# Performance work log

Measured on AMD Instinct MI355X. Metric: run time of the kernel, lower is better.

Reference implementation:

```python
import jax, jax.numpy as jnp
import numpy as np

# ---- module config (init_kwargs) ----
B, CIN, H, W_ = 2, 64, 56, 56
COUT, KH, KW = 128, 3, 3
K = CIN * KH * KW               # 576, reduction dim
ARRAY_ROWS = 128
IN_SLICES = (2, 2, 2, 2)        # 8-bit inputs, 2-bit slices
W_SLICES = (2, 2, 2, 2)         # 8-bit weights, 2-bit slices
N_STEPS_IN = 2 ** sum(IN_SLICES)    # 256, unsigned quantizer
N_STEPS_W = 2 ** sum(W_SLICES)      # 256
ADC_BINS = 256
ADC_STEP = 4.0

def _shifts_masks(slices):
    masks, shifts = [], [0]
    for s in slices[::-1]:
        masks.append((1 << s) - 1)
        shifts.append(s + shifts[-1])
    return np.array(shifts[-2::-1], np.int32), np.array(masks[::-1], np.int32)

_ish, _im = _shifts_masks(IN_SLICES)
_wsh, _wm = _shifts_masks(W_SLICES)
ISH, IM = jnp.asarray(_ish), jnp.asarray(_im)
WSH, WM = jnp.asarray(_wsh), jnp.asarray(_wm)
ISF = jnp.asarray((1 << _ish).astype(np.float32))  # slice recombine weights 2^shift
WSF = jnp.asarray((1 << _wsh).astype(np.float32))


def setup_inputs() -> dict:
    key = jax.random.key(0)
    k1, k2 = jax.random.split(key)
    return {
        "x": jax.random.normal(k1, (B, CIN, H, W_), jnp.float32),
        "w": jax.random.normal(k2, (COUT, CIN, KH, KW), jnp.float32),
    }


def _im2col(x):
    # 3x3 SAME conv patches, ordering [Cin, kh, kw] to match w.reshape(COUT, K)
    xp = jnp.pad(x, ((0, 0), (0, 0), (1, 1), (1, 1)))
    cols = jnp.stack([xp[:, :, i:i + H, j:j + W_]
                      for i in range(KH) for j in range(KW)], axis=2)  # [B,Cin,9,H,W]
    return cols.transpose(0, 3, 4, 1, 2).reshape(B * H * W_, K)  # [Nx, K]


def _quant_unsigned(v, n_steps):
    # Quantizer.offset + Quantizer.forward (unsigned, per-row over dim=-1)
    offs = v.min(axis=-1, keepdims=True)
    vr = v - offs
    step = vr.max(axis=-1, keepdims=True) / (n_steps - 1)
    q = jnp.round(jnp.clip(vr, 0.0, step * n_steps) / step).astype(jnp.int32)
    return q, step[..., 0], offs[..., 0]


def _slice_bits(q, shifts, masks):
    # Slicer.forward: stack (q >> shift) & mask along new leading slice dim
    s = shifts.reshape((-1,) + (1,) * q.ndim)
    m = masks.reshape((-1,) + (1,) * q.ndim)
    return (q[None] >> s) & m


def _chunk(t):
    # Chunker.forward over last dim K
    nb = -(-K // ARRAY_ROWS)
    npb = -(-K // nb)
    pad = nb * npb - K
    t = jnp.pad(t, [(0, 0)] * (t.ndim - 1) + [(0, pad)])
    t = t.reshape(t.shape[:-1] + (nb, npb))
    return jnp.moveaxis(t, -2, 0)  # [nb, ..., npb]


def reference(x, w):
    xf = _im2col(x)                    # [Nx, K]
    wf = w.reshape(COUT, K)            # [Ny, K]
    x_sum = xf.sum(axis=-1)            # [Nx]
    w_sum = wf.sum(axis=-1)            # [Ny]

    xq, x_scale, x_offs = _quant_unsigned(xf, N_STEPS_IN)
    wq, w_scale, w_offs = _quant_unsigned(wf, N_STEPS_W)

    xc = _chunk(_slice_bits(xq, ISH, IM))  # [nb, nis, Nx, npb] int32
    wc = _chunk(_slice_bits(wq, WSH, WM))  # [nb, nws, Ny, npb] int32

    # bit-serial crossbar MACs per (chunk, weight-slice, input-slice)
    z = jnp.einsum('bixk,bwyk->bwixy',
                   xc.astype(jnp.float32), wc.astype(jnp.float32))  # [nb,nws,nis,Nx,Ny]

    # ADC digitization (unsigned, fixed step): quantize then dequantize
    z = jnp.round(jnp.clip(z, 0.0, ADC_STEP * ADC_BINS) / ADC_STEP) * ADC_STEP

    # Chunker.reverse: sum crossbar blocks; Slicer.reverse: shift-weighted sums
    z = z.sum(axis=0)                               # [nws,nis,Nx,Ny]
    z = jnp.einsum('wixy,w,i->xy', z, WSF, ISF)     # [Nx,Ny]

    # dequantize scales and unsigned-offset correction:
    # x.y = sx*sy*(xq.yq) + x_offs*sum(y) + y_offs*sum(x) - x_offs*y_offs*K
    z = z * x_scale[:, None] * w_scale[None, :]
    z = (z + x_offs[:, None] * w_sum[None, :]
           + w_offs[None, :] * x_sum[:, None]
           - x_offs[:, None] * w_offs[None, :] * K)

    return z.reshape(B, H, W_, COUT).transpose(0, 3, 1, 2)  # [B,Cout,H,W]
```

## Files before the change

kernel.cpp:

```cpp
#include <hip/hip_runtime.h>


#define KDIM  576
#define NPB   116
#define SSTR  688

typedef int i32x4 __attribute__((ext_vector_type(4)));
typedef float f32x4 __attribute__((ext_vector_type(4)));

__device__ __forceinline__ i32x4 slice2b(i32x4 v, int sh) {
    i32x4 r;
    r[0] = (int)(((unsigned)v[0] >> sh) & 0x03030303u);
    r[1] = (int)(((unsigned)v[1] >> sh) & 0x03030303u);
    r[2] = (int)(((unsigned)v[2] >> sh) & 0x03030303u);
    r[3] = (int)(((unsigned)v[3] >> sh) & 0x03030303u);
    return r;
}

__device__ __forceinline__ void quant36(const float (&v)[36], unsigned char* rowp,
                                        int i16, float* sc, float* of,
                                        float* sm_, int sidx)
{
    float mn = v[0], mx = v[0], sm = 0.f;
#pragma unroll
    for (int m = 0; m < 36; m++) { mn = fminf(mn, v[m]); mx = fmaxf(mx, v[m]); sm += v[m]; }
#pragma unroll
    for (int off = 1; off < 16; off <<= 1) {
        mn = fminf(mn, __shfl_xor(mn, off));
        mx = fmaxf(mx, __shfl_xor(mx, off));
        sm += __shfl_xor(sm, off);
    }
    float step = (mx - mn) / 255.0f;
    if (i16 == 0) { sc[sidx] = step; of[sidx] = mn; sm_[sidx] = sm; }
    int k0 = i16 * 36;
#pragma unroll
    for (int d = 0; d < 9; d++) {
        unsigned int dw = 0;
#pragma unroll
        for (int mb = 0; mb < 4; mb++) {
            int q = (int)rintf((v[d * 4 + mb] - mn) / step);
            q = q < 0 ? 0 : (q > 255 ? 255 : q);
            dw |= (unsigned)q << (8 * mb);
        }
        int kd = k0 + d * 4;
        int ch = kd / NPB;
        *(unsigned int*)(rowp + kd + 12 * ch) = dw;
    }
}

__device__ __forceinline__ void zero_pads(unsigned char* scr, int tid) {
    int rl = tid >> 4, dwp = tid & 15;
    int col = dwp < 12 ? (dwp / 3) * 128 + 116 + (dwp % 3) * 4
                       : 624 + (dwp - 12) * 4;
    *(unsigned int*)(scr + rl * SSTR + col) = 0u;
}

__global__ __launch_bounds__(256) void k_wq(
    const float* __restrict__ w, unsigned char* __restrict__ Wq,
    float* __restrict__ wsc, float* __restrict__ wof, float* __restrict__ wsm)
{
    __shared__ __align__(16) unsigned char scrW[16 * SSTR];
    int tid = threadIdx.x, wv = tid >> 6, lane = tid & 63;
    int g = lane >> 4, i16 = lane & 15;
    int ctile = blockIdx.x;

    zero_pads(scrW, tid);
    __syncthreads();

    int rl = wv * 4 + g;
    int row = ctile * 16 + rl;
    const float* wr = w + (size_t)row * KDIM + i16 * 36;
    float v[36];
#pragma unroll
    for (int d = 0; d < 9; d++) {
        f32x4 t = *(const f32x4*)(wr + d * 4);
        v[d*4+0] = t[0]; v[d*4+1] = t[1]; v[d*4+2] = t[2]; v[d*4+3] = t[3];
    }
    quant36(v, scrW + rl * SSTR, i16, wsc, wof, wsm, row);
    __syncthreads();

    for (int idx = tid; idx < 640; idx += 256)
        *(i32x4*)(Wq + (size_t)ctile * 10240 + idx * 16) =
            *(const i32x4*)(scrW + (idx & 15) * SSTR + (idx >> 4) * 16);
}

__global__ __launch_bounds__(256) void k_main(
    const float* __restrict__ x, const unsigned char* __restrict__ Wq,
    const float* __restrict__ wscg, const float* __restrict__ wofg,
    const float* __restrict__ wsmg, float* __restrict__ out)
{
    __shared__ float xs2[64 * 57];
    __shared__ __align__(16) unsigned char scrX[16 * SSTR];
    __shared__ float xsc[16], xof[16], xsm[16];

    int tid = threadIdx.x, wv = tid >> 6, lane = tid & 63;
    int g = lane >> 4, i16 = lane & 15;
    int blk = blockIdx.x;
    int rtile = blk >> 1, chalf = blk & 1;
    int b = rtile >= 196 ? 1 : 0;
    int pos0 = (rtile - 196 * b) * 16;
    const float* xb = x + (size_t)(b * 64) * 3136;

    for (int i = tid; i < 64 * 54; i += 256) {
        int cin = i / 54, rem = i - cin * 54;
        int kh = rem / 18;
        int gg = pos0 + (rem - kh * 18) - 1;
        float vv = 0.f;
        if (gg >= 0 && gg < 3136) {
            int hg = gg / 56, wg = gg - hg * 56;
            int r = hg - 1 + kh;
            if (r >= 0 && r < 56) vv = xb[cin * 3136 + r * 56 + wg];
        }
        xs2[cin * 57 + rem] = vv;
    }
    zero_pads(scrX, tid);
    __syncthreads();

    {
        int i = wv * 4 + g;
        int pos = pos0 + i;
        int w_ = pos - (pos / 56) * 56;
        float v[36];
#pragma unroll
        for (int m = 0; m < 36; m++) {
            int r9 = m % 9, kh = r9 / 3, kw = r9 - kh * 3;
            int cin = i16 * 4 + m / 9;
            int ww = w_ - 1 + kw;
            v[m] = (ww >= 0 && ww < 56) ? xs2[cin * 57 + kh * 18 + i + kw] : 0.f;
        }
        quant36(v, scrX + i * SSTR, i16, xsc, xof, xsm, i);
    }
    __syncthreads();

    int ctl = chalf * 4 + wv;
    const unsigned char* Wg = Wq + (size_t)ctl * 10240;
    const unsigned char* xp = scrX + i16 * SSTR + g * 16;

    i32x4 acc = {0, 0, 0, 0};
    const i32x4 zero = {0, 0, 0, 0};

    for (int chunk = 0; chunk < 5; chunk++) {
        i32x4 ar0 = *(const i32x4*)(xp + chunk * 128);
        i32x4 ar1 = *(const i32x4*)(xp + chunk * 128 + 64);
        const i32x4* Wp = (const i32x4*)(Wg + chunk * 2048) + lane;
        i32x4 br0 = Wp[0], br1 = Wp[64];

        i32x4 wsl[4][2];
#pragma unroll
        for (int ws = 0; ws < 4; ws++) {
            wsl[ws][0] = slice2b(br0, 6 - 2 * ws);
            wsl[ws][1] = slice2b(br1, 6 - 2 * ws);
        }
#pragma unroll
        for (int is = 0; is < 4; is++) {
            int ish = 6 - 2 * is;
            i32x4 b0 = slice2b(ar0, ish);
            i32x4 b1 = slice2b(ar1, ish);
#pragma unroll
            for (int ws = 0; ws < 4; ws++) {
                i32x4 d = __builtin_amdgcn_mfma_i32_16x16x64_i8(wsl[ws][0], b0, zero, 0, 0, 0);
                d = __builtin_amdgcn_mfma_i32_16x16x64_i8(wsl[ws][1], b1, d, 0, 0, 0);
                int sh = ish + (6 - 2 * ws);
#pragma unroll
                for (int r = 0; r < 4; r++) {
                    int z = d[r];
                    z = z > 1024 ? 1024 : z;
                    int r4 = (z + 1 + ((z >> 2) & 1)) & ~3;
                    acc[r] += r4 << sh;
                }
            }
        }
    }

    float xs = xsc[i16], xo = xof[i16], xsmv = xsm[i16];
    int hw = pos0 + i16;
#pragma unroll
    for (int r = 0; r < 4; r++) {
        int wrow = ctl * 16 + g * 4 + r;
        float tt = ((float)acc[r] * xs) * wscg[wrow];
        float res = ((tt + xo * wsmg[wrow]) + wofg[wrow] * xsmv)
                  - (xo * wofg[wrow]) * 576.0f;
        out[(size_t)(b * 128 + wrow) * 3136 + hw] = res;
    }
}

extern "C" void kernel_launch(void* const* d_in, const int* in_sizes, int n_in,
                              void* d_out, int out_size, void* d_ws, size_t ws_size,
                              hipStream_t stream) {
    const float* x = (const float*)d_in[0];
    const float* w = (const float*)d_in[1];
    float* out = (float*)d_out;

    unsigned char* Wq = (unsigned char*)d_ws;
    float* wsc = (float*)(Wq + 81920);
    float* wof = wsc + 128;
    float* wsm = wof + 128;

    hipLaunchKernelGGL(k_wq, dim3(8), dim3(256), 0, stream, w, Wq, wsc, wof, wsm);
    hipLaunchKernelGGL(k_main, dim3(784), dim3(256), 0, stream,
                       x, Wq, wsc, wof, wsm, out);
}
```

Measured before the change: 40.00 us.

## Fuse weight quantization into main kernel and split K across waves

Removes the separate weight-quantization kernel launch. Each block now quantizes its own 32 weight rows into shared memory, reusing the input staging buffer. The grid grows to four output-channel quarters per row tile, and pairs of waves split the five K-chunks, combining partial sums through shared memory. Chunks are interleaved two at a time to raise MFMA independence. The cost is redundant weight loading and quantization in every block (1568 blocks, each rereading 32 rows of fp32 weights), plus an extra barrier.

```diff
diff --git a/kernel.cpp b/kernel.cpp
--- a/kernel.cpp
+++ b/kernel.cpp
@@ -17,6 +17,17 @@
     return r;
 }
 
+__device__ __forceinline__ void adc_acc(const i32x4 d, int sh, i32x4& acc) {
+#pragma unroll
+    for (int r = 0; r < 4; r++) {
+        int z = d[r];
+        z = z > 1024 ? 1024 : z;
+        int t = (z >> 2) & 1;
+        int r4 = (z + 1 + t) & ~3;
+        acc[r] += r4 << sh;
+    }
+}
+
 __device__ __forceinline__ void quant36(const float (&v)[36], unsigned char* rowp,
                                         int i16, float* sc, float* of,
                                         float* sm_, int sidx)
@@ -48,55 +59,95 @@
     }
 }
 
-__device__ __forceinline__ void zero_pads(unsigned char* scr, int tid) {
-    int rl = tid >> 4, dwp = tid & 15;
+__device__ __forceinline__ void zero_pad_row(unsigned char* scr, int idx) {
+    int rl = idx >> 4, dwp = idx & 15;
     int col = dwp < 12 ? (dwp / 3) * 128 + 116 + (dwp % 3) * 4
                        : 624 + (dwp - 12) * 4;
     *(unsigned int*)(scr + rl * SSTR + col) = 0u;
 }
 
-__global__ __launch_bounds__(256) void k_wq(
-    const float* __restrict__ w, unsigned char* __restrict__ Wq,
-    float* __restrict__ wsc, float* __restrict__ wof, float* __restrict__ wsm)
-{
-    __shared__ __align__(16) unsigned char scrW[16 * SSTR];
-    int tid = threadIdx.x, wv = tid >> 6, lane = tid & 63;
-    int g = lane >> 4, i16 = lane & 15;
-    int ctile = blockIdx.x;
-
-    zero_pads(scrW, tid);
-    __syncthreads();
-
-    int rl = wv * 4 + g;
-    int row = ctile * 16 + rl;
-    const float* wr = w + (size_t)row * KDIM + i16 * 36;
-    float v[36];
-#pragma unroll
-    for (int d = 0; d < 9; d++) {
-        f32x4 t = *(const f32x4*)(wr + d * 4);
-        v[d*4+0] = t[0]; v[d*4+1] = t[1]; v[d*4+2] = t[2]; v[d*4+3] = t[3];
-    }
-    quant36(v, scrW + rl * SSTR, i16, wsc, wof, wsm, row);
-    __syncthreads();
-
-    for (int idx = tid; idx < 640; idx += 256)
-        *(i32x4*)(Wq + (size_t)ctile * 10240 + idx * 16) =
-            *(const i32x4*)(scrW + (idx & 15) * SSTR + (idx >> 4) * 16);
-}
-
-__global__ __launch_bounds__(256) void k_main(
-    const float* __restrict__ x, const unsigned char* __restrict__ Wq,
-    const float* __restrict__ wscg, const float* __restrict__ wofg,
-    const float* __restrict__ wsmg, float* __restrict__ out)
-{
-    __shared__ float xs2[64 * 57];
+__device__ __forceinline__ void chunk1(const unsigned char* xp, const unsigned char* wp,
+                                       int ch, i32x4& acc)
+{
+    const i32x4 zero = {0, 0, 0, 0};
+    i32x4 x0 = *(const i32x4*)(xp + ch * 128);
+    i32x4 x1 = *(const i32x4*)(xp + ch * 128 + 64);
+    i32x4 w0 = *(const i32x4*)(wp + ch * 128);
+    i32x4 w1 = *(const i32x4*)(wp + ch * 128 + 64);
+    i32x4 ws0[4], ws1[4];
+#pragma unroll
+    for (int ws = 0; ws < 4; ws++) {
+        ws0[ws] = slice2b(w0, 6 - 2 * ws);
+        ws1[ws] = slice2b(w1, 6 - 2 * ws);
+    }
+#pragma unroll
+    for (int is = 0; is < 4; is++) {
+        int ish = 6 - 2 * is;
+        i32x4 a0 = slice2b(x0, ish), a1 = slice2b(x1, ish);
+#pragma unroll
+        for (int ws = 0; ws < 4; ws++) {
+            i32x4 d = __builtin_amdgcn_mfma_i32_16x16x64_i8(ws0[ws], a0, zero, 0, 0, 0);
+            d = __builtin_amdgcn_mfma_i32_16x16x64_i8(ws1[ws], a1, d, 0, 0, 0);
+            adc_acc(d, ish + 6 - 2 * ws, acc);
+        }
+    }
+}
+
+__device__ __forceinline__ void chunk2(const unsigned char* xp, const unsigned char* wp,
+                                       int ca, int cb, i32x4& acca, i32x4& accb)
+{
+    const i32x4 zero = {0, 0, 0, 0};
+    i32x4 xa0 = *(const i32x4*)(xp + ca * 128);
+    i32x4 xa1 = *(const i32x4*)(xp + ca * 128 + 64);
+    i32x4 xc0 = *(const i32x4*)(xp + cb * 128);
+    i32x4 xc1 = *(const i32x4*)(xp + cb * 128 + 64);
+    i32x4 wa0 = *(const i32x4*)(wp + ca * 128);
+    i32x4 wa1 = *(const i32x4*)(wp + ca * 128 + 64);
+    i32x4 wc0 = *(const i32x4*)(wp + cb * 128);
+    i32x4 wc1 = *(const i32x4*)(wp + cb * 128 + 64);
+    i32x4 wsa0[4], wsa1[4], wsb0[4], wsb1[4];
+#pragma unroll
+    for (int ws = 0; ws < 4; ws++) {
+        wsa0[ws] = slice2b(wa0, 6 - 2 * ws);
+        wsa1[ws] = slice2b(wa1, 6 - 2 * ws);
+        wsb0[ws] = slice2b(wc0, 6 - 2 * ws);
+        wsb1[ws] = slice2b(wc1, 6 - 2 * ws);
+    }
+#pragma unroll
+    for (int is = 0; is < 4; is++) {
+        int ish = 6 - 2 * is;
+        i32x4 a0 = slice2b(xa0, ish), a1 = slice2b(xa1, ish);
+        i32x4 b0 = slice2b(xc0, ish), b1 = slice2b(xc1, ish);
+#pragma unroll
+        for (int ws = 0; ws < 4; ws++) {
+            i32x4 da = __builtin_amdgcn_mfma_i32_16x16x64_i8(wsa0[ws], a0, zero, 0, 0, 0);
+            i32x4 db = __builtin_amdgcn_mfma_i32_16x16x64_i8(wsb0[ws], b0, zero, 0, 0, 0);
+            da = __builtin_amdgcn_mfma_i32_16x16x64_i8(wsa1[ws], a1, da, 0, 0, 0);
+            db = __builtin_amdgcn_mfma_i32_16x16x64_i8(wsb1[ws], b1, db, 0, 0, 0);
+            int sh = ish + 6 - 2 * ws;
+            adc_acc(da, sh, acca);
+            adc_acc(db, sh, accb);
+        }
+    }
+}
+
+__global__ __launch_bounds__(256, 4) void k_one(
+    const float* __restrict__ x, const float* __restrict__ w,
+    float* __restrict__ out)
+{
     __shared__ __align__(16) unsigned char scrX[16 * SSTR];
+    __shared__ __align__(16) unsigned char uni[32 * SSTR];
+    __shared__ __align__(16) int pacc[2][64][4];
     __shared__ float xsc[16], xof[16], xsm[16];
+    __shared__ float wscl[32], wofl[32], wsml[32];
+
+    float* xs2 = (float*)uni;
+    unsigned char* scrW = uni;
 
     int tid = threadIdx.x, wv = tid >> 6, lane = tid & 63;
     int g = lane >> 4, i16 = lane & 15;
     int blk = blockIdx.x;
-    int rtile = blk >> 1, chalf = blk & 1;
+    int rtile = blk >> 2, cq = blk & 3;
     int b = rtile >= 196 ? 1 : 0;
     int pos0 = (rtile - 196 * b) * 16;
     const float* xb = x + (size_t)(b * 64) * 3136;
@@ -113,7 +164,7 @@
         }
         xs2[cin * 57 + rem] = vv;
     }
-    zero_pads(scrX, tid);
+    zero_pad_row(scrX, tid);
     __syncthreads();
 
     {
@@ -132,55 +183,61 @@
     }
     __syncthreads();
 
-    int ctl = chalf * 4 + wv;
-    const unsigned char* Wg = Wq + (size_t)ctl * 10240;
+    for (int idx = tid; idx < 512; idx += 256) zero_pad_row(scrW, idx);
+    {
+        int g16 = wv * 4 + g;
+#pragma unroll
+        for (int q = 0; q < 2; q++) {
+            int rl = g16 * 2 + q;
+            int row = cq * 32 + rl;
+            const float* wr = w + (size_t)row * KDIM + i16 * 36;
+            float v[36];
+#pragma unroll
+            for (int d = 0; d < 9; d++) {
+                f32x4 t = *(const f32x4*)(wr + d * 4);
+                v[d*4+0] = t[0]; v[d*4+1] = t[1]; v[d*4+2] = t[2]; v[d*4+3] = t[3];
+            }
+            quant36(v, scrW + rl * SSTR, i16, wscl, wofl, wsml, rl);
+        }
+    }
+    __syncthreads();
+
+    int ctl_l = wv >> 1, khalf = wv & 1;
     const unsigned char* xp = scrX + i16 * SSTR + g * 16;
+    const unsigned char* wp = scrW + (ctl_l * 16 + i16) * SSTR + g * 16;
 
     i32x4 acc = {0, 0, 0, 0};
-    const i32x4 zero = {0, 0, 0, 0};
-
-    for (int chunk = 0; chunk < 5; chunk++) {
-        i32x4 ar0 = *(const i32x4*)(xp + chunk * 128);
-        i32x4 ar1 = *(const i32x4*)(xp + chunk * 128 + 64);
-        const i32x4* Wp = (const i32x4*)(Wg + chunk * 2048) + lane;
-        i32x4 br0 = Wp[0], br1 = Wp[64];
-
-        i32x4 wsl[4][2];
-#pragma unroll
-        for (int ws = 0; ws < 4; ws++) {
-            wsl[ws][0] = slice2b(br0, 6 - 2 * ws);
-            wsl[ws][1] = slice2b(br1, 6 - 2 * ws);
-        }
-#pragma unroll
-        for (int is = 0; is < 4; is++) {
-            int ish = 6 - 2 * is;
-            i32x4 b0 = slice2b(ar0, ish);
-            i32x4 b1 = slice2b(ar1, ish);
-#pragma unroll
-            for (int ws = 0; ws < 4; ws++) {
-                i32x4 d = __builtin_amdgcn_mfma_i32_16x16x64_i8(wsl[ws][0], b0, zero, 0, 0, 0);
-                d = __builtin_amdgcn_mfma_i32_16x16x64_i8(wsl[ws][1], b1, d, 0, 0, 0);
-                int sh = ish + (6 - 2 * ws);
-#pragma unroll
-                for (int r = 0; r < 4; r++) {
-                    int z = d[r];
-                    z = z > 1024 ? 1024 : z;
-                    int r4 = (z + 1 + ((z >> 2) & 1)) & ~3;
-                    acc[r] += r4 << sh;
-                }
-            }
-        }
-    }
-
-    float xs = xsc[i16], xo = xof[i16], xsmv = xsm[i16];
-    int hw = pos0 + i16;
-#pragma unroll
-    for (int r = 0; r < 4; r++) {
-        int wrow = ctl * 16 + g * 4 + r;
-        float tt = ((float)acc[r] * xs) * wscg[wrow];
-        float res = ((tt + xo * wsmg[wrow]) + wofg[wrow] * xsmv)
-                  - (xo * wofg[wrow]) * 576.0f;
-        out[(size_t)(b * 128 + wrow) * 3136 + hw] = res;
+    if (khalf == 0) {
+        i32x4 acc2 = {0, 0, 0, 0};
+        chunk2(xp, wp, 0, 1, acc, acc2);
+        chunk1(xp, wp, 2, acc);
+#pragma unroll
+        for (int r = 0; r < 4; r++) acc[r] += acc2[r];
+        *(i32x4*)&pacc[ctl_l][lane][0] = acc;
+    } else {
+        i32x4 acc2 = {0, 0, 0, 0};
+        chunk2(xp, wp, 3, 4, acc, acc2);
+#pragma unroll
+        for (int r = 0; r < 4; r++) acc[r] += acc2[r];
+    }
+    __syncthreads();
+
+    if (khalf == 1) {
+        i32x4 p = *(const i32x4*)&pacc[ctl_l][lane][0];
+#pragma unroll
+        for (int r = 0; r < 4; r++) acc[r] += p[r];
+
+        float xs_ = xsc[i16], xo = xof[i16], xsv = xsm[i16];
+        int hw = pos0 + i16;
+#pragma unroll
+        for (int r = 0; r < 4; r++) {
+            int rl = ctl_l * 16 + g * 4 + r;
+            int wrow = cq * 32 + rl;
+            float tt = ((float)acc[r] * xs_) * wscl[rl];
+            float res = ((tt + xo * wsml[rl]) + wofl[rl] * xsv)
+                      - (xo * wofl[rl]) * 576.0f;
+            out[(size_t)(b * 128 + wrow) * 3136 + hw] = res;
+        }
     }
 }
 
@@ -191,12 +248,5 @@
     const float* w = (const float*)d_in[1];
     float* out = (float*)d_out;
 
-    unsigned char* Wq = (unsigned char*)d_ws;
-    float* wsc = (float*)(Wq + 81920);
-    float* wof = wsc + 128;
-    float* wsm = wof + 128;
-
-    hipLaunchKernelGGL(k_wq, dim3(8), dim3(256), 0, stream, w, Wq, wsc, wof, wsm);
-    hipLaunchKernelGGL(k_main, dim3(784), dim3(256), 0, stream,
-                       x, Wq, wsc, wof, wsm, out);
-}
+    hipLaunchKernelGGL(k_one, dim3(1568), dim3(256), 0, stream, x, w, out);
+}
```

Result: slower. 57.83 us (+44.6%).

## Split input quantization into its own pass and split K across waves in the MFMA kernel

Applied to the files above, without the earlier changes.

Before, every row tile quantized its input patches twice, once per output-channel half. Now a single quantization kernel quantizes each input tile once, alongside the weights, and writes both to workspace in an MFMA-friendly layout. A second kernel has each block cover 2 row tiles by 1 column tile, with waves splitting the 5 K-chunks 3/2 and reducing through shared memory. Independent accumulators per weight slice shorten dependency chains. The cost is extra global traffic for the quantized inputs and an uneven K split between waves.

```diff
diff --git a/kernel.cpp b/kernel.cpp
--- a/kernel.cpp
+++ b/kernel.cpp
@@ -48,75 +48,54 @@
     }
 }
 
-__device__ __forceinline__ void zero_pads(unsigned char* scr, int tid) {
-    int rl = tid >> 4, dwp = tid & 15;
+__device__ __forceinline__ void zero_pad_row(unsigned char* scr, int idx) {
+    int rl = idx >> 4, dwp = idx & 15;
     int col = dwp < 12 ? (dwp / 3) * 128 + 116 + (dwp % 3) * 4
                        : 624 + (dwp - 12) * 4;
     *(unsigned int*)(scr + rl * SSTR + col) = 0u;
 }
 
-__global__ __launch_bounds__(256) void k_wq(
-    const float* __restrict__ w, unsigned char* __restrict__ Wq,
-    float* __restrict__ wsc, float* __restrict__ wof, float* __restrict__ wsm)
-{
-    __shared__ __align__(16) unsigned char scrW[16 * SSTR];
-    int tid = threadIdx.x, wv = tid >> 6, lane = tid & 63;
-    int g = lane >> 4, i16 = lane & 15;
-    int ctile = blockIdx.x;
-
-    zero_pads(scrW, tid);
-    __syncthreads();
-
-    int rl = wv * 4 + g;
-    int row = ctile * 16 + rl;
-    const float* wr = w + (size_t)row * KDIM + i16 * 36;
-    float v[36];
-#pragma unroll
-    for (int d = 0; d < 9; d++) {
-        f32x4 t = *(const f32x4*)(wr + d * 4);
-        v[d*4+0] = t[0]; v[d*4+1] = t[1]; v[d*4+2] = t[2]; v[d*4+3] = t[3];
-    }
-    quant36(v, scrW + rl * SSTR, i16, wsc, wof, wsm, row);
-    __syncthreads();
-
-    for (int idx = tid; idx < 640; idx += 256)
-        *(i32x4*)(Wq + (size_t)ctile * 10240 + idx * 16) =
-            *(const i32x4*)(scrW + (idx & 15) * SSTR + (idx >> 4) * 16);
-}
-
-__global__ __launch_bounds__(256) void k_main(
-    const float* __restrict__ x, const unsigned char* __restrict__ Wq,
-    const float* __restrict__ wscg, const float* __restrict__ wofg,
-    const float* __restrict__ wsmg, float* __restrict__ out)
+__device__ __forceinline__ void copy_out(const unsigned char* scr,
+                                         unsigned char* dst, int tid) {
+    for (int idx = tid; idx < 640; idx += 256) {
+        int u = idx >> 4, rl = idx & 15;
+        int dst16 = (u >> 3) * 128 + ((u >> 2) & 1) * 64 + (u & 3) * 16 + rl;
+        *(i32x4*)(dst + dst16 * 16) = *(const i32x4*)(scr + rl * SSTR + u * 16);
+    }
+}
+
+__global__ __launch_bounds__(256) void k_q(
+    const float* __restrict__ x, const float* __restrict__ w,
+    unsigned char* __restrict__ Xq, unsigned char* __restrict__ Wq,
+    float* __restrict__ xscg, float* __restrict__ xofg, float* __restrict__ xsmg,
+    float* __restrict__ wscg, float* __restrict__ wofg, float* __restrict__ wsmg)
 {
     __shared__ float xs2[64 * 57];
-    __shared__ __align__(16) unsigned char scrX[16 * SSTR];
-    __shared__ float xsc[16], xof[16], xsm[16];
+    __shared__ __align__(16) unsigned char scr[16 * SSTR];
 
     int tid = threadIdx.x, wv = tid >> 6, lane = tid & 63;
     int g = lane >> 4, i16 = lane & 15;
     int blk = blockIdx.x;
-    int rtile = blk >> 1, chalf = blk & 1;
-    int b = rtile >= 196 ? 1 : 0;
-    int pos0 = (rtile - 196 * b) * 16;
-    const float* xb = x + (size_t)(b * 64) * 3136;
-
-    for (int i = tid; i < 64 * 54; i += 256) {
-        int cin = i / 54, rem = i - cin * 54;
-        int kh = rem / 18;
-        int gg = pos0 + (rem - kh * 18) - 1;
-        float vv = 0.f;
-        if (gg >= 0 && gg < 3136) {
-            int hg = gg / 56, wg = gg - hg * 56;
-            int r = hg - 1 + kh;
-            if (r >= 0 && r < 56) vv = xb[cin * 3136 + r * 56 + wg];
-        }
-        xs2[cin * 57 + rem] = vv;
-    }
-    zero_pads(scrX, tid);
-    __syncthreads();
-
-    {
+
+    if (blk < 392) {
+        int b = blk >= 196 ? 1 : 0;
+        int pos0 = (blk - 196 * b) * 16;
+        const float* xb = x + (size_t)(b * 64) * 3136;
+        for (int i = tid; i < 64 * 54; i += 256) {
+            int cin = i / 54, rem = i - cin * 54;
+            int kh = rem / 18;
+            int gg = pos0 + (rem - kh * 18) - 1;
+            float vv = 0.f;
+            if (gg >= 0 && gg < 3136) {
+                int hg = gg / 56, wg = gg - hg * 56;
+                int r = hg - 1 + kh;
+                if (r >= 0 && r < 56) vv = xb[cin * 3136 + r * 56 + wg];
+            }
+            xs2[cin * 57 + rem] = vv;
+        }
+        zero_pad_row(scr, tid);
+        __syncthreads();
+
         int i = wv * 4 + g;
         int pos = pos0 + i;
         int w_ = pos - (pos / 56) * 56;
@@ -128,59 +107,116 @@
             int ww = w_ - 1 + kw;
             v[m] = (ww >= 0 && ww < 56) ? xs2[cin * 57 + kh * 18 + i + kw] : 0.f;
         }
-        quant36(v, scrX + i * SSTR, i16, xsc, xof, xsm, i);
-    }
+        quant36(v, scr + i * SSTR, i16, xscg, xofg, xsmg, blk * 16 + i);
+        __syncthreads();
+
+        copy_out(scr, Xq + (size_t)blk * 10240, tid);
+    } else {
+        int ctile = blk - 392;
+        zero_pad_row(scr, tid);
+        int rl = wv * 4 + g;
+        int row = ctile * 16 + rl;
+        const float* wr = w + (size_t)row * KDIM + i16 * 36;
+        float v[36];
+#pragma unroll
+        for (int d = 0; d < 9; d++) {
+            f32x4 t = *(const f32x4*)(wr + d * 4);
+            v[d*4+0] = t[0]; v[d*4+1] = t[1]; v[d*4+2] = t[2]; v[d*4+3] = t[3];
+        }
+        quant36(v, scr + rl * SSTR, i16, wscg, wofg, wsmg, row);
+        __syncthreads();
+
+        copy_out(scr, Wq + (size_t)ctile * 10240, tid);
+    }
+}
+
+__device__ __forceinline__ void chunk_ws(const unsigned char* xt, const unsigned char* wt,
+                                         int ch, int lane, i32x4 (&acc4)[4])
+{
+    const i32x4 zero = {0, 0, 0, 0};
+    i32x4 x0 = *(const i32x4*)(xt + ch * 2048 + lane * 16);
+    i32x4 x1 = *(const i32x4*)(xt + ch * 2048 + 1024 + lane * 16);
+    i32x4 w0 = *(const i32x4*)(wt + ch * 2048 + lane * 16);
+    i32x4 w1 = *(const i32x4*)(wt + ch * 2048 + 1024 + lane * 16);
+    i32x4 ws0[4], ws1[4];
+#pragma unroll
+    for (int ws = 0; ws < 4; ws++) {
+        ws0[ws] = slice2b(w0, 6 - 2 * ws);
+        ws1[ws] = slice2b(w1, 6 - 2 * ws);
+    }
+#pragma unroll
+    for (int is = 0; is < 4; is++) {
+        int ish = 6 - 2 * is;
+        i32x4 a0 = slice2b(x0, ish), a1 = slice2b(x1, ish);
+#pragma unroll
+        for (int ws = 0; ws < 4; ws++) {
+            i32x4 d = __builtin_amdgcn_mfma_i32_16x16x64_i8(ws0[ws], a0, zero, 0, 0, 0);
+            d = __builtin_amdgcn_mfma_i32_16x16x64_i8(ws1[ws], a1, d, 0, 0, 0);
+            int sh = ish + 6 - 2 * ws;
+#pragma unroll
+            for (int r = 0; r < 4; r++) {
+                int z = d[r];
+                z = z > 1024 ? 1024 : z;
+                int t = (z >> 2) & 1;
+                int r4 = (z + 1 + t) & ~3;
+                acc4[ws][r] += r4 << sh;
+            }
+        }
+    }
+}
+
+__global__ __launch_bounds__(256) void k_d(
+    const unsigned char* __restrict__ Xq, const unsigned char* __restrict__ Wq,
+    const float* __restrict__ xscg, const float* __restrict__ xofg,
+    const float* __restrict__ xsmg,
+    const float* __restrict__ wscg, const float* __restrict__ wofg,
+    const float* __restrict__ wsmg, float* __restrict__ out)
+{
+    __shared__ __align__(16) int pacc[2][64][4];
+
+    int tid = threadIdx.x, wv = tid >> 6, lane = tid & 63;
+    int g = lane >> 4, i16 = lane & 15;
+    int blk = blockIdx.x;
+    int ct = blk & 7, rp = blk >> 3;
+    int tl = wv & 1, khalf = wv >> 1;
+    int rtile = rp * 2 + tl;
+    const unsigned char* xt = Xq + (size_t)rtile * 10240;
+    const unsigned char* wt = Wq + (size_t)ct * 10240;
+
+    i32x4 acc4[4] = {{0,0,0,0},{0,0,0,0},{0,0,0,0},{0,0,0,0}};
+    if (khalf == 0) {
+        chunk_ws(xt, wt, 0, lane, acc4);
+        chunk_ws(xt, wt, 1, lane, acc4);
+        chunk_ws(xt, wt, 2, lane, acc4);
+    } else {
+        chunk_ws(xt, wt, 3, lane, acc4);
+        chunk_ws(xt, wt, 4, lane, acc4);
+    }
+    i32x4 acc;
+#pragma unroll
+    for (int r = 0; r < 4; r++)
+        acc[r] = (acc4[0][r] + acc4[1][r]) + (acc4[2][r] + acc4[3][r]);
+
+    if (khalf == 0) *(i32x4*)&pacc[tl][lane][0] = acc;
     __syncthreads();
 
-    int ctl = chalf * 4 + wv;
-    const unsigned char* Wg = Wq + (size_t)ctl * 10240;
-    const unsigned char* xp = scrX + i16 * SSTR + g * 16;
-
-    i32x4 acc = {0, 0, 0, 0};
-    const i32x4 zero = {0, 0, 0, 0};
-
-    for (int chunk = 0; chunk < 5; chunk++) {
-        i32x4 ar0 = *(const i32x4*)(xp + chunk * 128);
-        i32x4 ar1 = *(const i32x4*)(xp + chunk * 128 + 64);
-        const i32x4* Wp = (const i32x4*)(Wg + chunk * 2048) + lane;
-        i32x4 br0 = Wp[0], br1 = Wp[64];
-
-        i32x4 wsl[4][2];
-#pragma unroll
-        for (int ws = 0; ws < 4; ws++) {
-            wsl[ws][0] = slice2b(br0, 6 - 2 * ws);
-            wsl[ws][1] = slice2b(br1, 6 - 2 * ws);
-        }
-#pragma unroll
-        for (int is = 0; is < 4; is++) {
-            int ish = 6 - 2 * is;
-            i32x4 b0 = slice2b(ar0, ish);
-            i32x4 b1 = slice2b(ar1, ish);
-#pragma unroll
-            for (int ws = 0; ws < 4; ws++) {
-                i32x4 d = __builtin_amdgcn_mfma_i32_16x16x64_i8(wsl[ws][0], b0, zero, 0, 0, 0);
-                d = __builtin_amdgcn_mfma_i32_16x16x64_i8(wsl[ws][1], b1, d, 0, 0, 0);
-                int sh = ish + (6 - 2 * ws);
-#pragma unroll
-                for (int r = 0; r < 4; r++) {
-                    int z = d[r];
-                    z = z > 1024 ? 1024 : z;
-                    int r4 = (z + 1 + ((z >> 2) & 1)) & ~3;
-                    acc[r] += r4 << sh;
-                }
-            }
-        }
-    }
-
-    float xs = xsc[i16], xo = xof[i16], xsmv = xsm[i16];
-    int hw = pos0 + i16;
-#pragma unroll
-    for (int r = 0; r < 4; r++) {
-        int wrow = ctl * 16 + g * 4 + r;
-        float tt = ((float)acc[r] * xs) * wscg[wrow];
-        float res = ((tt + xo * wsmg[wrow]) + wofg[wrow] * xsmv)
-                  - (xo * wofg[wrow]) * 576.0f;
-        out[(size_t)(b * 128 + wrow) * 3136 + hw] = res;
+    if (khalf == 1) {
+        i32x4 p = *(const i32x4*)&pacc[tl][lane][0];
+#pragma unroll
+        for (int r = 0; r < 4; r++) acc[r] += p[r];
+
+        int b = rtile >= 196 ? 1 : 0;
+        int xrow = rtile * 16 + i16;
+        float xs_ = xscg[xrow], xo = xofg[xrow], xsv = xsmg[xrow];
+        int hw = (rtile - 196 * b) * 16 + i16;
+#pragma unroll
+        for (int r = 0; r < 4; r++) {
+            int wrow = ct * 16 + g * 4 + r;
+            float tt = ((float)acc[r] * xs_) * wscg[wrow];
+            float res = ((tt + xo * wsmg[wrow]) + wofg[wrow] * xsv)
+                      - (xo * wofg[wrow]) * 576.0f;
+            out[(size_t)(b * 128 + wrow) * 3136 + hw] = res;
+        }
     }
 }
 
@@ -191,12 +227,17 @@
     const float* w = (const float*)d_in[1];
     float* out = (float*)d_out;
 
-    unsigned char* Wq = (unsigned char*)d_ws;
-    float* wsc = (float*)(Wq + 81920);
+    unsigned char* Xq = (unsigned char*)d_ws;
+    unsigned char* Wq = Xq + (size_t)392 * 10240;
+    float* xsc = (float*)(Wq + 8 * 10240);
+    float* xof = xsc + 6272;
+    float* xsm = xof + 6272;
+    float* wsc = xsm + 6272;
     float* wof = wsc + 128;
     float* wsm = wof + 128;
 
-    hipLaunchKernelGGL(k_wq, dim3(8), dim3(256), 0, stream, w, Wq, wsc, wof, wsm);
-    hipLaunchKernelGGL(k_main, dim3(784), dim3(256), 0, stream,
-                       x, Wq, wsc, wof, wsm, out);
-}
+    hipLaunchKernelGGL(k_q, dim3(400), dim3(256), 0, stream,
+                       x, w, Xq, Wq, xsc, xof, xsm, wsc, wof, wsm);
+    hipLaunchKernelGGL(k_d, dim3(1568), dim3(256), 0, stream,
+                       Xq, Wq, xsc, xof, xsm, wsc, wof, wsm, out);
+}
```

New measurement: 37.12 us. -7.2%, faster.
